# Kernel tuning notes

Hardware: AMD Instinct MI355X
Metric: run time of the kernel (lower is better)

## Reference

```python
import jax, jax.numpy as jnp
from jax import lax
from jax.scipy.special import logsumexp
import numpy as np

N_NODES = 6144
N_EDGES = 98304
N_FEAT = 128
N_TPLT = 16
M_NODES = 10
N_CG = 5        # conditional-gradient (Frank-Wolfe) outer iterations
N_SINK = 50     # log-domain Sinkhorn iterations for the linearized OT subproblem


def setup_inputs() -> dict:
    key = jax.random.key(0)
    k1, k2, k3, k4 = jax.random.split(key, 4)
    x = jax.random.normal(k1, (N_NODES, N_FEAT), dtype=jnp.float32)
    edge_index = jax.random.randint(k2, (2, N_EDGES), 0, N_NODES, dtype=jnp.int64)
    # template_initialisation: uniform(0,1) adjacencies, symmetrized; normal features; zero q0/alpha0
    t_raw = jax.random.uniform(k3, (N_TPLT, M_NODES, M_NODES), dtype=jnp.float32)
    templates = 0.5 * (t_raw + jnp.transpose(t_raw, (0, 2, 1)))
    templates_features = jax.random.normal(k4, (N_TPLT, M_NODES, N_FEAT), dtype=jnp.float32)
    q0 = jnp.zeros((N_TPLT, M_NODES), dtype=jnp.float32)
    alpha0 = jnp.zeros((1,), dtype=jnp.float32)
    return {"x": x, "edge_index": edge_index, "templates": templates,
            "templates_features": templates_features, "q0": q0, "alpha0": alpha0}


def _sinkhorn_log(G, logp, logq, reg):
    """Log-domain Sinkhorn solving min <G,T> + reg*H(T) over U(p,q)."""
    K = -G / reg                         # [n, m]
    f0 = jnp.zeros_like(logp)

    def body(f, _):
        g = logq - logsumexp(K + f[:, None], axis=0)
        f = logp - logsumexp(K + g[None, :], axis=1)
        return f, None

    f, _ = lax.scan(body, f0, None, length=N_SINK)
    g = logq - logsumexp(K + f[:, None], axis=0)
    return jnp.exp(f[:, None] + K + g[None, :])


def _fgw2(M, C1, C2, p, q, alpha):
    """Fused Gromov-Wasserstein distance (square loss) via conditional gradient.
    M: [n,m] feature cost, C1: [n,n] graph structure, C2: [m,m] template structure."""
    # init_matrix (square loss): constC = f1(C1) p 1^T + 1 q^T f2(C2)^T
    constC = (C1 ** 2 @ p)[:, None] + (C2 ** 2 @ q)[None, :]   # [n, m]
    logp, logq = jnp.log(p), jnp.log(q)
    T0 = p[:, None] * q[None, :]

    def step(T, _):
        C1TC2 = C1 @ T @ C2                                   # [n, m] (dominant cost)
        grad = (1.0 - alpha) * M + alpha * 2.0 * (constC - 2.0 * C1TC2)
        reg = lax.stop_gradient(0.05 * jnp.max(jnp.abs(grad)) + 1e-8)
        Tn = _sinkhorn_log(grad, logp, logq, reg)             # linearized OT subproblem
        dT = Tn - T
        # exact line search for the quadratic objective along dT
        C1dTC2 = C1 @ dT @ C2
        a = -2.0 * alpha * jnp.sum(C1dTC2 * dT)
        b = (1.0 - alpha) * jnp.sum(M * dT) + alpha * (jnp.sum(constC * dT) - 4.0 * jnp.sum(C1TC2 * dT))
        tau = jnp.where(a > 0.0,
                        jnp.clip(-b / (2.0 * a + 1e-16), 0.0, 1.0),
                        jnp.where(a + b < 0.0, 1.0, 0.0))
        return T + tau * dT, None

    T, _ = lax.scan(step, T0, None, length=N_CG)
    gw = jnp.sum((constC - 2.0 * (C1 @ T @ C2)) * T)
    wass = jnp.sum(M * T)
    return (1.0 - alpha) * wass + alpha * gw


def reference(x, edge_index, templates, templates_features, q0, alpha0):
    alpha = jax.nn.sigmoid(alpha0)[0]
    q = jax.nn.softmax(q0, axis=1)                            # [T, m] template node weights
    n = x.shape[0]
    # dense adjacency from edge list (symmetrized)
    A = jnp.zeros((n, n), dtype=x.dtype).at[edge_index[0], edge_index[1]].set(1.0)
    C1 = jnp.maximum(A, A.T)                                  # [n, n]
    p = jnp.full((n,), 1.0 / n, dtype=x.dtype)
    # squared euclidean feature cost per template: [T, n, m]
    M = (jnp.sum(x ** 2, axis=1)[None, :, None]
         + jnp.sum(templates_features ** 2, axis=-1)[:, None, :]
         - 2.0 * jnp.einsum('nf,tmf->tnm', x, templates_features))
    dists = jax.vmap(_fgw2, in_axes=(0, None, 0, None, 0, None))(M, C1, templates, p, q, alpha)
    return dists                                              # [n_templates]
```

## Files before the change

kernel.cpp:

```cpp
#include <hip/hip_runtime.h>
#include <hip/hip_cooperative_groups.h>

namespace cgx = cooperative_groups;

static constexpr int NN  = 6144;
static constexpr int NE  = 98304;
static constexpr int NF  = 128;
static constexpr int NT  = 16;
static constexpr int MN  = 10;
static constexpr int NCG = 5;
static constexpr int NSK = 50;
static constexpr int WPR = NN / 32;
static constexpr int TPB = 768;
static constexpr int NBLK = 256;
static constexpr int RPT = NN / TPB;
static constexpr int NW  = TPB / 64;

static_assert(TPB * RPT == NN, "row mapping");

static constexpr size_t OFF_M   = 0;
static constexpr size_t OFF_T   = OFF_M  + (size_t)NT * NN * MN;
static constexpr size_t OFF_C   = OFF_T  + (size_t)NT * NN * 5;
static constexpr size_t OFF_D   = OFF_C  + (size_t)NT * NN * 5;
static constexpr size_t OFF_RS  = OFF_D  + (size_t)NT * NN * 5;
static constexpr size_t OFF_DEG = OFF_RS + NN;
static constexpr size_t OFF_CI  = OFF_DEG + NN;
static constexpr size_t OFF_NNZ = OFF_CI + NE;

static constexpr int LDS_PL  = NN * 20;
static constexpr int LDS_SP  = TPB * 7 * 4;
static constexpr int LDS_DYN = LDS_PL + LDS_SP;

__device__ __forceinline__ unsigned f2bf(float f) {
    unsigned u = __float_as_uint(f);
    return (u + 0x7fffu + ((u >> 16) & 1u)) >> 16;
}
__device__ __forceinline__ unsigned packbf(float a, float b) { return f2bf(a) | (f2bf(b) << 16); }
__device__ __forceinline__ float bflo(unsigned w) { return __uint_as_float(w << 16); }
__device__ __forceinline__ float bfhi(unsigned w) { return __uint_as_float(w & 0xffff0000u); }

extern __shared__ char sMem[];

__global__ __launch_bounds__(TPB) void tfgw_kernel(
    const float* __restrict__ x, const void* __restrict__ eiv,
    const float* __restrict__ tpl, const float* __restrict__ tf,
    const float* __restrict__ q0, const float* __restrict__ a0,
    float* __restrict__ out, float* __restrict__ W)
{
    __shared__ float sC2[MN * MN];
    __shared__ float sq[MN], scq[MN], sqC2[MN], sNSQ[MN];
    __shared__ unsigned svp[5];
    __shared__ float sVf[MN];
    __shared__ float sCv[5];
    __shared__ float sRed[3 * NW];
    __shared__ float sBC[2];
    __shared__ float sDots[4];

    const int tid = threadIdx.x;
    const int bid = blockIdx.x;

    unsigned* BM    = (unsigned*)(W + OFF_T);
    int* rowst      = (int*)(W + OFF_RS);
    int* degi       = (int*)(W + OFF_DEG);
    unsigned short* colix = (unsigned short*)(W + OFF_CI);
    int* nnzc       = (int*)(W + OFF_NNZ);
    float* Mw  = W + OFF_M;
    unsigned* Tg = (unsigned*)(W + OFF_T);
    unsigned* Cg = (unsigned*)(W + OFF_C);
    unsigned* Dg = (unsigned*)(W + OFF_D);

    uint4*    PL4x = (uint4*)sMem;
    unsigned* PL1x = (unsigned*)(sMem + NN * 16);
    unsigned* sPp  = (unsigned*)(sMem + LDS_PL);

    const float alpha  = 1.f / (1.f + __expf(-a0[0]));
    const float invn   = 1.f / (float)NN;
    const float alpha2 = 2.f * alpha;
    const float oma    = 1.f - alpha;

    cgx::grid_group grid = cgx::this_grid();

    for (int idx = bid * TPB + tid; idx < NN * WPR; idx += NBLK * TPB) BM[idx] = 0u;
    if (bid == 0 && tid == 0) *nnzc = 0;
    grid.sync();

    {
        const unsigned* uw = (const unsigned*)eiv;
        const bool is64 = (uw[1] == 0u && uw[3] == 0u && uw[5] == 0u);
        for (int e = bid * TPB + tid; e < NE; e += NBLK * TPB) {
            int s, d;
            if (is64) {
                s = (int)((const long long*)eiv)[e];
                d = (int)((const long long*)eiv)[NE + e];
            } else {
                s = ((const int*)eiv)[e];
                d = ((const int*)eiv)[NE + e];
            }
            atomicOr(&BM[(size_t)s * WPR + (d >> 5)], 1u << (d & 31));
            atomicOr(&BM[(size_t)d * WPR + (s >> 5)], 1u << (s & 31));
        }
        float* sTF = (float*)sMem;
        const int t = bid >> 4, rb = bid & 15;
        for (int k = tid; k < MN * NF; k += TPB) sTF[k] = tf[t * MN * NF + k];
        __syncthreads();
        if (tid < MN) {
            float s = 0.f;
            for (int k = 0; k < NF; ++k) { float v = sTF[tid * NF + k]; s += v * v; }
            sNSQ[tid] = s;
        }
        __syncthreads();
        if (tid < 384) {
            const int i = rb * 384 + tid;
            const float4* x4 = (const float4*)(x + (size_t)i * NF);
            const float4* t4 = (const float4*)sTF;
            float acc[MN]; float xn = 0.f;
            #pragma unroll
            for (int j = 0; j < MN; ++j) acc[j] = 0.f;
            for (int k4 = 0; k4 < NF / 4; ++k4) {
                float4 xv = x4[k4];
                xn += xv.x * xv.x + xv.y * xv.y + xv.z * xv.z + xv.w * xv.w;
                #pragma unroll
                for (int j = 0; j < MN; ++j) {
                    float4 tv = t4[j * (NF / 4) + k4];
                    acc[j] += xv.x * tv.x + xv.y * tv.y + xv.z * tv.z + xv.w * tv.w;
                }
            }
            float* Mrow = Mw + (size_t)t * NN * MN + (size_t)i * MN;
            #pragma unroll
            for (int j = 0; j < MN; ++j) Mrow[j] = xn + sNSQ[j] - 2.f * acc[j];
        }
    }
    grid.sync();

    {
        const int i = bid * TPB + tid;
        if (i < NN) {
            int cnt = 0;
            for (int w = 0; w < WPR; ++w) cnt += __popc(BM[(size_t)i * WPR + w]);
            int st = atomicAdd(nnzc, cnt);
            rowst[i] = st; degi[i] = cnt;
            int p = st;
            for (int w = 0; w < WPR; ++w) {
                unsigned m = BM[(size_t)i * WPR + w];
                while (m) { int b = __ffs(m) - 1; m &= m - 1; colix[p++] = (unsigned short)((w << 5) + b); }
            }
        }
    }
    grid.sync();

    if (bid >= NT) return;

    const int t = bid;
    float* Mb = Mw + (size_t)t * NN * MN;
    unsigned* Tb = Tg + (size_t)t * NN * 5;
    unsigned* Cb = Cg + (size_t)t * NN * 5;
    unsigned* Db = Dg + (size_t)t * NN * 5;

    if (tid == 0) {
        float qv[MN]; float qm = -1e30f;
        for (int j = 0; j < MN; ++j) { qv[j] = q0[t * MN + j]; qm = fmaxf(qm, qv[j]); }
        float qs = 0.f;
        for (int j = 0; j < MN; ++j) { qv[j] = __expf(qv[j] - qm); qs += qv[j]; }
        for (int j = 0; j < MN; ++j) { qv[j] /= qs; sq[j] = qv[j]; }
        for (int j = 0; j < MN; ++j) {
            float s2 = 0.f, s1 = 0.f;
            for (int k = 0; k < MN; ++k) {
                float cjk = tpl[t * MN * MN + j * MN + k];
                s2 += cjk * cjk * qv[k];
                s1 += tpl[t * MN * MN + k * MN + j] * qv[k];
            }
            scq[j] = s2; sqC2[j] = s1;
        }
    }
    for (int k = tid; k < MN * MN; k += TPB) sC2[k] = tpl[t * MN * MN + k];
    __syncthreads();

    float uu[RPT];

    for (int cgi = 0; cgi < NCG; ++cgi) {
        if (tid == 0) {
            float tau = 0.f;
            if (cgi > 0) {
                float a = -2.f * alpha * sDots[3];
                float b = oma * sDots[0] + alpha * (sDots[1] - 4.f * sDots[2]);
                if (a > 0.f) tau = fminf(fmaxf(-b / (2.f * a + 1e-16f), 0.f), 1.f);
                else         tau = (a + b < 0.f) ? 1.f : 0.f;
            }
            sBC[0] = tau;
        }
        __syncthreads();
        const float tau = sBC[0];
        if (cgi > 0 && tau == 0.f) break;

        float gmax = 0.f;
        #pragma unroll
        for (int k = 0; k < RPT; ++k) {
            const int r = tid + k * TPB;
            const float cp = (float)degi[r] * invn;
            const size_t b5 = (size_t)r * 5;
            float C[MN];
            if (cgi == 0) {
                #pragma unroll
                for (int h = 0; h < 5; ++h) {
                    unsigned tw = packbf(sq[2*h] * invn, sq[2*h+1] * invn);
                    unsigned cw = packbf(cp * sqC2[2*h], cp * sqC2[2*h+1]);
                    Tb[b5 + h] = tw; Cb[b5 + h] = cw;
                    C[2*h] = bflo(cw); C[2*h+1] = bfhi(cw);
                }
            } else {
                float dd[MN];
                uint4 a = PL4x[r]; unsigned b4 = PL1x[r];
                dd[0]=bflo(a.x); dd[1]=bfhi(a.x); dd[2]=bflo(a.y); dd[3]=bfhi(a.y);
                dd[4]=bflo(a.z); dd[5]=bfhi(a.z); dd[6]=bflo(a.w); dd[7]=bfhi(a.w);
                dd[8]=bflo(b4);  dd[9]=bfhi(b4);
                #pragma unroll
                for (int h = 0; h < 5; ++h) {
                    unsigned tw = Tb[b5 + h], cw = Cb[b5 + h], Dw = Db[b5 + h];
                    float T0 = bflo(tw) + tau * dd[2*h];
                    float T1 = bfhi(tw) + tau * dd[2*h+1];
                    float C0 = bflo(cw) + tau * bflo(Dw);
                    float C1v = bfhi(cw) + tau * bfhi(Dw);
                    unsigned ntw = packbf(T0, T1), ncw = packbf(C0, C1v);
                    Tb[b5 + h] = ntw; Cb[b5 + h] = ncw;
                    C[2*h] = bflo(ncw); C[2*h+1] = bfhi(ncw);
                }
            }
            float g[MN];
            #pragma unroll
            for (int h = 0; h < 5; ++h) {
                float2 mv = *(const float2*)(Mb + (size_t)r * MN + 2*h);
                g[2*h]   = oma * mv.x + alpha2 * (cp + scq[2*h]   - 2.f * C[2*h]);
                g[2*h+1] = oma * mv.y + alpha2 * (cp + scq[2*h+1] - 2.f * C[2*h+1]);
                gmax = fmaxf(gmax, fmaxf(__builtin_fabsf(g[2*h]), __builtin_fabsf(g[2*h+1])));
            }
            PL4x[r] = make_uint4(packbf(g[0],g[1]), packbf(g[2],g[3]),
                                 packbf(g[4],g[5]), packbf(g[6],g[7]));
            PL1x[r] = packbf(g[8], g[9]);
        }
        #pragma unroll
        for (int d = 32; d; d >>= 1) gmax = fmaxf(gmax, __shfl_xor(gmax, d));
        if ((tid & 63) == 0) sRed[tid >> 6] = gmax;
        __syncthreads();
        if (tid == 0) {
            float m = sRed[0];
            for (int w = 1; w < NW; ++w) m = fmaxf(m, sRed[w]);
            sBC[1] = 1.f / (0.05f * m + 1e-8f);
        }
        __syncthreads();
        const float invreg = sBC[1];

        #pragma unroll
        for (int k = 0; k < RPT; ++k) {
            const int r = tid + k * TPB;
            uint4 a = PL4x[r]; unsigned b4 = PL1x[r];
            float g[MN];
            g[0]=bflo(a.x); g[1]=bfhi(a.x); g[2]=bflo(a.y); g[3]=bfhi(a.y);
            g[4]=bflo(a.z); g[5]=bfhi(a.z); g[6]=bflo(a.w); g[7]=bfhi(a.w);
            g[8]=bflo(b4);  g[9]=bfhi(b4);
            float e[MN];
            #pragma unroll
            for (int j = 0; j < MN; ++j) e[j] = __expf(-g[j] * invreg);
            PL4x[r] = make_uint4(packbf(e[0],e[1]), packbf(e[2],e[3]),
                                 packbf(e[4],e[5]), packbf(e[6],e[7]));
            PL1x[r] = packbf(e[8], e[9]);
        }

        if (cgi == 0) {
            float a[MN];
            #pragma unroll
            for (int j = 0; j < MN; ++j) a[j] = 0.f;
            #pragma unroll
            for (int k = 0; k < RPT; ++k) {
                const int r = tid + k * TPB;
                uint4 q = PL4x[r]; unsigned b4 = PL1x[r];
                a[0]+=bflo(q.x); a[1]+=bfhi(q.x); a[2]+=bflo(q.y); a[3]+=bfhi(q.y);
                a[4]+=bflo(q.z); a[5]+=bfhi(q.z); a[6]+=bflo(q.w); a[7]+=bfhi(q.w);
                a[8]+=bflo(b4);  a[9]+=bfhi(b4);
            }
            #pragma unroll
            for (int p = 0; p < 5; ++p) sPp[tid * 7 + p] = packbf(a[2*p], a[2*p+1]);
            __syncthreads();
            if (tid < 320) {
                const int p = tid >> 6, c = tid & 63;
                float s0 = 0.f, s1 = 0.f;
                #pragma unroll
                for (int kk = 0; kk < NW; ++kk) {
                    unsigned w = sPp[(c + (kk << 6)) * 7 + p];
                    s0 += bflo(w); s1 += bfhi(w);
                }
                #pragma unroll
                for (int d = 32; d; d >>= 1) { s0 += __shfl_xor(s0, d); s1 += __shfl_xor(s1, d); }
                if (c == 0) {
                    float v0 = sq[2*p] / s0, v1 = sq[2*p+1] / s1;
                    svp[p] = packbf(v0, v1);
                    sVf[2*p] = v0; sVf[2*p+1] = v1;
                }
            }
            __syncthreads();
        }

        for (int it = 1; it <= NSK; ++it) {
            float vv[MN];
            #pragma unroll
            for (int p = 0; p < 5; ++p) {
                unsigned w = svp[p];
                vv[2*p] = bflo(w); vv[2*p+1] = bfhi(w);
            }
            float a[MN];
            #pragma unroll
            for (int j = 0; j < MN; ++j) a[j] = 0.f;
            #pragma unroll
            for (int k = 0; k < RPT; ++k) {
                const int r = tid + k * TPB;
                uint4 q = PL4x[r]; unsigned b4 = PL1x[r];
                float e[MN];
                e[0]=bflo(q.x); e[1]=bfhi(q.x); e[2]=bflo(q.y); e[3]=bfhi(q.y);
                e[4]=bflo(q.z); e[5]=bfhi(q.z); e[6]=bflo(q.w); e[7]=bfhi(q.w);
                e[8]=bflo(b4);  e[9]=bfhi(b4);
                float R = 0.f;
                #pragma unroll
                for (int j = 0; j < MN; ++j) R += e[j] * vv[j];
                const float u = invn * __builtin_amdgcn_rcpf(R);
                uu[k] = u;
                #pragma unroll
                for (int j = 0; j < MN; ++j) a[j] += e[j] * u;
            }
            #pragma unroll
            for (int p = 0; p < 5; ++p) sPp[tid * 7 + p] = packbf(a[2*p], a[2*p+1]);
            __syncthreads();
            if (tid < 320) {
                const int p = tid >> 6, c = tid & 63;
                float s0 = 0.f, s1 = 0.f;
                #pragma unroll
                for (int kk = 0; kk < NW; ++kk) {
                    unsigned w = sPp[(c + (kk << 6)) * 7 + p];
                    s0 += bflo(w); s1 += bfhi(w);
                }
                #pragma unroll
                for (int d = 32; d; d >>= 1) { s0 += __shfl_xor(s0, d); s1 += __shfl_xor(s1, d); }
                if (c == 0) {
                    float v0 = sq[2*p] / s0, v1 = sq[2*p+1] / s1;
                    float o0 = sVf[2*p],    o1 = sVf[2*p+1];
                    sCv[p] = (__builtin_fabsf(v0 - o0) <= 2e-4f * v0 &&
                              __builtin_fabsf(v1 - o1) <= 2e-4f * v1) ? 1.f : 0.f;
                    sVf[2*p] = v0; sVf[2*p+1] = v1;
                    svp[p] = packbf(v0, v1);
                }
            }
            __syncthreads();
            if (sCv[0] + sCv[1] + sCv[2] + sCv[3] + sCv[4] == 5.f) break;
        }

        {
            float vv[MN];
            #pragma unroll
            for (int p = 0; p < 5; ++p) {
                unsigned w = svp[p];
                vv[2*p] = bflo(w); vv[2*p+1] = bfhi(w);
            }
            float sMdT = 0.f, sCdT = 0.f, sCTdT = 0.f;
            #pragma unroll
            for (int k = 0; k < RPT; ++k) {
                const int r = tid + k * TPB;
                const float cp = (float)degi[r] * invn;
                const size_t b5 = (size_t)r * 5;
                const float u = uu[k];
                uint4 q = PL4x[r]; unsigned b4 = PL1x[r];
                float e[MN], dd[MN];
                e[0]=bflo(q.x); e[1]=bfhi(q.x); e[2]=bflo(q.y); e[3]=bfhi(q.y);
                e[4]=bflo(q.z); e[5]=bfhi(q.z); e[6]=bflo(q.w); e[7]=bfhi(q.w);
                e[8]=bflo(b4);  e[9]=bfhi(b4);
                #pragma unroll
                for (int h = 0; h < 5; ++h) {
                    unsigned tw = Tb[b5 + h], cw = Cb[b5 + h];
                    float2 mv = *(const float2*)(Mb + (size_t)r * MN + 2*h);
                    float d0 = u * e[2*h]   * vv[2*h]   - bflo(tw);
                    float d1 = u * e[2*h+1] * vv[2*h+1] - bfhi(tw);
                    dd[2*h] = d0; dd[2*h+1] = d1;
                    sMdT  += mv.x * d0 + mv.y * d1;
                    sCdT  += (cp + scq[2*h]) * d0 + (cp + scq[2*h+1]) * d1;
                    sCTdT += bflo(cw) * d0 + bfhi(cw) * d1;
                }
                PL4x[r] = make_uint4(packbf(dd[0],dd[1]), packbf(dd[2],dd[3]),
                                     packbf(dd[4],dd[5]), packbf(dd[6],dd[7]));
                PL1x[r] = packbf(dd[8], dd[9]);
            }
            #pragma unroll
            for (int d = 32; d; d >>= 1) {
                sMdT  += __shfl_xor(sMdT, d);
                sCdT  += __shfl_xor(sCdT, d);
                sCTdT += __shfl_xor(sCTdT, d);
            }
            if ((tid & 63) == 0) {
                const int w = tid >> 6;
                sRed[w] = sMdT; sRed[NW + w] = sCdT; sRed[2*NW + w] = sCTdT;
            }
            __syncthreads();
            if (tid == 0) {
                float r0 = 0.f, r1 = 0.f, r2 = 0.f;
                for (int w = 0; w < NW; ++w) { r0 += sRed[w]; r1 += sRed[NW+w]; r2 += sRed[2*NW+w]; }
                sDots[0] = r0; sDots[1] = r1; sDots[2] = r2;
            }
        }

        {
            float dot = 0.f;
            #pragma unroll
            for (int k = 0; k < RPT; ++k) {
                const int r = tid + k * TPB;
                float y[MN];
                #pragma unroll
                for (int j = 0; j < MN; ++j) y[j] = 0.f;
                const int st = rowst[r], dg = degi[r];
                const unsigned short* cl = colix + st;
                for (int e = 0; e < dg; ++e) {
                    const int j = cl[e];
                    uint4 q = PL4x[j]; unsigned b4 = PL1x[j];
                    y[0] += bflo(q.x); y[1] += bfhi(q.x);
                    y[2] += bflo(q.y); y[3] += bfhi(q.y);
                    y[4] += bflo(q.z); y[5] += bfhi(q.z);
                    y[6] += bflo(q.w); y[7] += bfhi(q.w);
                    y[8] += bflo(b4);  y[9] += bfhi(b4);
                }
                uint4 q = PL4x[r]; unsigned b4 = PL1x[r];
                float dd[MN];
                dd[0]=bflo(q.x); dd[1]=bfhi(q.x); dd[2]=bflo(q.y); dd[3]=bfhi(q.y);
                dd[4]=bflo(q.z); dd[5]=bfhi(q.z); dd[6]=bflo(q.w); dd[7]=bfhi(q.w);
                dd[8]=bflo(b4);  dd[9]=bfhi(b4);
                #pragma unroll
                for (int h = 0; h < 5; ++h) {
                    float o0 = 0.f, o1 = 0.f;
                    #pragma unroll
                    for (int j = 0; j < MN; ++j) {
                        o0 += y[j] * sC2[j * MN + 2*h];
                        o1 += y[j] * sC2[j * MN + 2*h + 1];
                    }
                    dot += o0 * dd[2*h] + o1 * dd[2*h+1];
                    Db[(size_t)r * 5 + h] = packbf(o0, o1);
                }
            }
            #pragma unroll
            for (int d = 32; d; d >>= 1) dot += __shfl_xor(dot, d);
            if ((tid & 63) == 0) sRed[tid >> 6] = dot;
            __syncthreads();
            if (tid == 0) {
                float s = 0.f;
                for (int w = 0; w < NW; ++w) s += sRed[w];
                sDots[3] = s;
            }
            __syncthreads();
        }
    }

    if (tid == 0) {
        float a = -2.f * alpha * sDots[3];
        float b = oma * sDots[0] + alpha * (sDots[1] - 4.f * sDots[2]);
        float tau;
        if (a > 0.f) tau = fminf(fmaxf(-b / (2.f * a + 1e-16f), 0.f), 1.f);
        else         tau = (a + b < 0.f) ? 1.f : 0.f;
        sBC[0] = tau;
    }
    __syncthreads();
    {
        const float tau = sBC[0];
        float gw = 0.f, wass = 0.f;
        #pragma unroll
        for (int k = 0; k < RPT; ++k) {
            const int r = tid + k * TPB;
            const float cp = (float)degi[r] * invn;
            const size_t b5 = (size_t)r * 5;
            uint4 q = PL4x[r]; unsigned b4 = PL1x[r];
            float dd[MN];
            dd[0]=bflo(q.x); dd[1]=bfhi(q.x); dd[2]=bflo(q.y); dd[3]=bfhi(q.y);
            dd[4]=bflo(q.z); dd[5]=bfhi(q.z); dd[6]=bflo(q.w); dd[7]=bfhi(q.w);
            dd[8]=bflo(b4);  dd[9]=bfhi(b4);
            #pragma unroll
            for (int h = 0; h < 5; ++h) {
                unsigned tw = Tb[b5 + h], cw = Cb[b5 + h], Dw = Db[b5 + h];
                float2 mv = *(const float2*)(Mb + (size_t)r * MN + 2*h);
                float Tf0 = bflo(tw) + tau * dd[2*h];
                float Tf1 = bfhi(tw) + tau * dd[2*h+1];
                float Cf0 = bflo(cw) + tau * bflo(Dw);
                float Cf1 = bfhi(cw) + tau * bfhi(Dw);
                gw   += (cp + scq[2*h]   - 2.f * Cf0) * Tf0
                      + (cp + scq[2*h+1] - 2.f * Cf1) * Tf1;
                wass += mv.x * Tf0 + mv.y * Tf1;
            }
        }
        #pragma unroll
        for (int d = 32; d; d >>= 1) {
            gw   += __shfl_xor(gw, d);
            wass += __shfl_xor(wass, d);
        }
        if ((tid & 63) == 0) { sRed[tid >> 6] = gw; sRed[NW + (tid >> 6)] = wass; }
        __syncthreads();
        if (tid == 0) {
            float g = 0.f, ws = 0.f;
            for (int w = 0; w < NW; ++w) { g += sRed[w]; ws += sRed[NW + w]; }
            out[t] = oma * ws + alpha * g;
        }
    }
}

extern "C" void kernel_launch(void* const* d_in, const int* in_sizes, int n_in,
                              void* d_out, int out_size, void* d_ws, size_t ws_size,
                              hipStream_t stream) {
    const float* x   = (const float*)d_in[0];
    const void*  ei  = d_in[1];
    const float* tpl = (const float*)d_in[2];
    const float* tfp = (const float*)d_in[3];
    const float* q0  = (const float*)d_in[4];
    const float* a0  = (const float*)d_in[5];
    float* outp = (float*)d_out;
    float* Wp   = (float*)d_ws;
    (void)hipFuncSetAttribute(reinterpret_cast<const void*>(&tfgw_kernel),
                              hipFuncAttributeMaxDynamicSharedMemorySize, LDS_DYN);
    void* args[] = { &x, &ei, &tpl, &tfp, &q0, &a0, &outp, &Wp };
    hipLaunchCooperativeKernel(reinterpret_cast<const void*>(&tfgw_kernel),
                               dim3(NBLK), dim3(TPB), args, LDS_DYN, stream);
}
```

Before: 706.6 us.

## Split T/C/D global buffers into uint4+uint planes and recompute Sinkhorn row scale

Stores the per-template bf16 T, C and D arrays as a 16-byte uint4 plane plus a 4-byte plane, instead of five strided 4-byte words per row. Loads and stores become coalesced vector accesses rather than stride-20 scalar ones. The Sinkhorn row scale u is recomputed in the direction pass instead of being kept in a register array, which lowers register pressure. The convergence test now compares packed bf16 column scalings against the previous two iterates instead of using a float relative tolerance, which may change when Sinkhorn stops early.

```diff
diff --git a/kernel.cpp b/kernel.cpp
--- a/kernel.cpp
+++ b/kernel.cpp
@@ -19,10 +19,13 @@
 static_assert(TPB * RPT == NN, "row mapping");
 
 static constexpr size_t OFF_M   = 0;
-static constexpr size_t OFF_T   = OFF_M  + (size_t)NT * NN * MN;
-static constexpr size_t OFF_C   = OFF_T  + (size_t)NT * NN * 5;
-static constexpr size_t OFF_D   = OFF_C  + (size_t)NT * NN * 5;
-static constexpr size_t OFF_RS  = OFF_D  + (size_t)NT * NN * 5;
+static constexpr size_t OFF_T4  = OFF_M  + (size_t)NT * NN * MN;
+static constexpr size_t OFF_T1  = OFF_T4 + (size_t)NT * NN * 4;
+static constexpr size_t OFF_C4  = OFF_T1 + (size_t)NT * NN;
+static constexpr size_t OFF_C1  = OFF_C4 + (size_t)NT * NN * 4;
+static constexpr size_t OFF_D4  = OFF_C1 + (size_t)NT * NN;
+static constexpr size_t OFF_D1  = OFF_D4 + (size_t)NT * NN * 4;
+static constexpr size_t OFF_RS  = OFF_D1 + (size_t)NT * NN;
 static constexpr size_t OFF_DEG = OFF_RS + NN;
 static constexpr size_t OFF_CI  = OFF_DEG + NN;
 static constexpr size_t OFF_NNZ = OFF_CI + NE;
@@ -50,7 +53,7 @@
     __shared__ float sC2[MN * MN];
     __shared__ float sq[MN], scq[MN], sqC2[MN], sNSQ[MN];
     __shared__ unsigned svp[5];
-    __shared__ float sVf[MN];
+    __shared__ unsigned svP2[5];
     __shared__ float sCv[5];
     __shared__ float sRed[3 * NW];
     __shared__ float sBC[2];
@@ -59,15 +62,12 @@
     const int tid = threadIdx.x;
     const int bid = blockIdx.x;
 
-    unsigned* BM    = (unsigned*)(W + OFF_T);
+    unsigned* BM    = (unsigned*)(W + OFF_T4);
     int* rowst      = (int*)(W + OFF_RS);
     int* degi       = (int*)(W + OFF_DEG);
     unsigned short* colix = (unsigned short*)(W + OFF_CI);
     int* nnzc       = (int*)(W + OFF_NNZ);
     float* Mw  = W + OFF_M;
-    unsigned* Tg = (unsigned*)(W + OFF_T);
-    unsigned* Cg = (unsigned*)(W + OFF_C);
-    unsigned* Dg = (unsigned*)(W + OFF_D);
 
     uint4*    PL4x = (uint4*)sMem;
     unsigned* PL1x = (unsigned*)(sMem + NN * 16);
@@ -152,9 +152,12 @@
 
     const int t = bid;
     float* Mb = Mw + (size_t)t * NN * MN;
-    unsigned* Tb = Tg + (size_t)t * NN * 5;
-    unsigned* Cb = Cg + (size_t)t * NN * 5;
-    unsigned* Db = Dg + (size_t)t * NN * 5;
+    uint4*    Tb4 = (uint4*)(W + OFF_T4) + (size_t)t * NN;
+    unsigned* Tb1 = (unsigned*)(W + OFF_T1) + (size_t)t * NN;
+    uint4*    Cb4 = (uint4*)(W + OFF_C4) + (size_t)t * NN;
+    unsigned* Cb1 = (unsigned*)(W + OFF_C1) + (size_t)t * NN;
+    uint4*    Db4 = (uint4*)(W + OFF_D4) + (size_t)t * NN;
+    unsigned* Db1 = (unsigned*)(W + OFF_D1) + (size_t)t * NN;
 
     if (tid == 0) {
         float qv[MN]; float qm = -1e30f;
@@ -175,8 +178,6 @@
     for (int k = tid; k < MN * MN; k += TPB) sC2[k] = tpl[t * MN * MN + k];
     __syncthreads();
 
-    float uu[RPT];
-
     for (int cgi = 0; cgi < NCG; ++cgi) {
         if (tid == 0) {
             float tau = 0.f;
@@ -188,6 +189,7 @@
             }
             sBC[0] = tau;
         }
+        if (tid < 5) svP2[tid] = 0xFFFFFFFFu;
         __syncthreads();
         const float tau = sBC[0];
         if (cgi > 0 && tau == 0.f) break;
@@ -197,33 +199,52 @@
         for (int k = 0; k < RPT; ++k) {
             const int r = tid + k * TPB;
             const float cp = (float)degi[r] * invn;
-            const size_t b5 = (size_t)r * 5;
             float C[MN];
             if (cgi == 0) {
-                #pragma unroll
-                for (int h = 0; h < 5; ++h) {
-                    unsigned tw = packbf(sq[2*h] * invn, sq[2*h+1] * invn);
-                    unsigned cw = packbf(cp * sqC2[2*h], cp * sqC2[2*h+1]);
-                    Tb[b5 + h] = tw; Cb[b5 + h] = cw;
-                    C[2*h] = bflo(cw); C[2*h+1] = bfhi(cw);
-                }
+                uint4 tw4; unsigned tw1;
+                uint4 cw4; unsigned cw1;
+                tw4.x = packbf(sq[0]*invn, sq[1]*invn); tw4.y = packbf(sq[2]*invn, sq[3]*invn);
+                tw4.z = packbf(sq[4]*invn, sq[5]*invn); tw4.w = packbf(sq[6]*invn, sq[7]*invn);
+                tw1   = packbf(sq[8]*invn, sq[9]*invn);
+                cw4.x = packbf(cp*sqC2[0], cp*sqC2[1]); cw4.y = packbf(cp*sqC2[2], cp*sqC2[3]);
+                cw4.z = packbf(cp*sqC2[4], cp*sqC2[5]); cw4.w = packbf(cp*sqC2[6], cp*sqC2[7]);
+                cw1   = packbf(cp*sqC2[8], cp*sqC2[9]);
+                Tb4[r] = tw4; Tb1[r] = tw1; Cb4[r] = cw4; Cb1[r] = cw1;
+                C[0]=bflo(cw4.x); C[1]=bfhi(cw4.x); C[2]=bflo(cw4.y); C[3]=bfhi(cw4.y);
+                C[4]=bflo(cw4.z); C[5]=bfhi(cw4.z); C[6]=bflo(cw4.w); C[7]=bfhi(cw4.w);
+                C[8]=bflo(cw1);   C[9]=bfhi(cw1);
             } else {
                 float dd[MN];
                 uint4 a = PL4x[r]; unsigned b4 = PL1x[r];
                 dd[0]=bflo(a.x); dd[1]=bfhi(a.x); dd[2]=bflo(a.y); dd[3]=bfhi(a.y);
                 dd[4]=bflo(a.z); dd[5]=bfhi(a.z); dd[6]=bflo(a.w); dd[7]=bfhi(a.w);
                 dd[8]=bflo(b4);  dd[9]=bfhi(b4);
-                #pragma unroll
-                for (int h = 0; h < 5; ++h) {
-                    unsigned tw = Tb[b5 + h], cw = Cb[b5 + h], Dw = Db[b5 + h];
-                    float T0 = bflo(tw) + tau * dd[2*h];
-                    float T1 = bfhi(tw) + tau * dd[2*h+1];
-                    float C0 = bflo(cw) + tau * bflo(Dw);
-                    float C1v = bfhi(cw) + tau * bfhi(Dw);
-                    unsigned ntw = packbf(T0, T1), ncw = packbf(C0, C1v);
-                    Tb[b5 + h] = ntw; Cb[b5 + h] = ncw;
-                    C[2*h] = bflo(ncw); C[2*h+1] = bfhi(ncw);
-                }
+                uint4 tw4 = Tb4[r]; unsigned tw1 = Tb1[r];
+                uint4 cw4 = Cb4[r]; unsigned cw1 = Cb1[r];
+                uint4 Dw4 = Db4[r]; unsigned Dw1 = Db1[r];
+                float T[MN], Dd[MN];
+                T[0]=bflo(tw4.x); T[1]=bfhi(tw4.x); T[2]=bflo(tw4.y); T[3]=bfhi(tw4.y);
+                T[4]=bflo(tw4.z); T[5]=bfhi(tw4.z); T[6]=bflo(tw4.w); T[7]=bfhi(tw4.w);
+                T[8]=bflo(tw1);   T[9]=bfhi(tw1);
+                C[0]=bflo(cw4.x); C[1]=bfhi(cw4.x); C[2]=bflo(cw4.y); C[3]=bfhi(cw4.y);
+                C[4]=bflo(cw4.z); C[5]=bfhi(cw4.z); C[6]=bflo(cw4.w); C[7]=bfhi(cw4.w);
+                C[8]=bflo(cw1);   C[9]=bfhi(cw1);
+                Dd[0]=bflo(Dw4.x); Dd[1]=bfhi(Dw4.x); Dd[2]=bflo(Dw4.y); Dd[3]=bfhi(Dw4.y);
+                Dd[4]=bflo(Dw4.z); Dd[5]=bfhi(Dw4.z); Dd[6]=bflo(Dw4.w); Dd[7]=bfhi(Dw4.w);
+                Dd[8]=bflo(Dw1);   Dd[9]=bfhi(Dw1);
+                #pragma unroll
+                for (int j = 0; j < MN; ++j) { T[j] += tau * dd[j]; C[j] += tau * Dd[j]; }
+                uint4 ntw4; unsigned ntw1; uint4 ncw4; unsigned ncw1;
+                ntw4.x = packbf(T[0],T[1]); ntw4.y = packbf(T[2],T[3]);
+                ntw4.z = packbf(T[4],T[5]); ntw4.w = packbf(T[6],T[7]);
+                ntw1   = packbf(T[8],T[9]);
+                ncw4.x = packbf(C[0],C[1]); ncw4.y = packbf(C[2],C[3]);
+                ncw4.z = packbf(C[4],C[5]); ncw4.w = packbf(C[6],C[7]);
+                ncw1   = packbf(C[8],C[9]);
+                Tb4[r] = ntw4; Tb1[r] = ntw1; Cb4[r] = ncw4; Cb1[r] = ncw1;
+                C[0]=bflo(ncw4.x); C[1]=bfhi(ncw4.x); C[2]=bflo(ncw4.y); C[3]=bfhi(ncw4.y);
+                C[4]=bflo(ncw4.z); C[5]=bfhi(ncw4.z); C[6]=bflo(ncw4.w); C[7]=bfhi(ncw4.w);
+                C[8]=bflo(ncw1);   C[9]=bfhi(ncw1);
             }
             float g[MN];
             #pragma unroll
@@ -290,11 +311,7 @@
                 }
                 #pragma unroll
                 for (int d = 32; d; d >>= 1) { s0 += __shfl_xor(s0, d); s1 += __shfl_xor(s1, d); }
-                if (c == 0) {
-                    float v0 = sq[2*p] / s0, v1 = sq[2*p+1] / s1;
-                    svp[p] = packbf(v0, v1);
-                    sVf[2*p] = v0; sVf[2*p+1] = v1;
-                }
+                if (c == 0) svp[p] = packbf(sq[2*p] / s0, sq[2*p+1] / s1);
             }
             __syncthreads();
         }
@@ -321,7 +338,6 @@
                 #pragma unroll
                 for (int j = 0; j < MN; ++j) R += e[j] * vv[j];
                 const float u = invn * __builtin_amdgcn_rcpf(R);
-                uu[k] = u;
                 #pragma unroll
                 for (int j = 0; j < MN; ++j) a[j] += e[j] * u;
             }
@@ -339,12 +355,11 @@
                 #pragma unroll
                 for (int d = 32; d; d >>= 1) { s0 += __shfl_xor(s0, d); s1 += __shfl_xor(s1, d); }
                 if (c == 0) {
-                    float v0 = sq[2*p] / s0, v1 = sq[2*p+1] / s1;
-                    float o0 = sVf[2*p],    o1 = sVf[2*p+1];
-                    sCv[p] = (__builtin_fabsf(v0 - o0) <= 2e-4f * v0 &&
-                              __builtin_fabsf(v1 - o1) <= 2e-4f * v1) ? 1.f : 0.f;
-                    sVf[2*p] = v0; sVf[2*p+1] = v1;
-                    svp[p] = packbf(v0, v1);
+                    unsigned pw = packbf(sq[2*p] / s0, sq[2*p+1] / s1);
+                    unsigned old = svp[p], old2 = svP2[p];
+                    sCv[p] = (pw == old || pw == old2) ? 1.f : 0.f;
+                    svP2[p] = old;
+                    svp[p] = pw;
                 }
             }
             __syncthreads();
@@ -363,23 +378,33 @@
             for (int k = 0; k < RPT; ++k) {
                 const int r = tid + k * TPB;
                 const float cp = (float)degi[r] * invn;
-                const size_t b5 = (size_t)r * 5;
-                const float u = uu[k];
                 uint4 q = PL4x[r]; unsigned b4 = PL1x[r];
                 float e[MN], dd[MN];
                 e[0]=bflo(q.x); e[1]=bfhi(q.x); e[2]=bflo(q.y); e[3]=bfhi(q.y);
                 e[4]=bflo(q.z); e[5]=bfhi(q.z); e[6]=bflo(q.w); e[7]=bfhi(q.w);
                 e[8]=bflo(b4);  e[9]=bfhi(b4);
+                float R = 0.f;
+                #pragma unroll
+                for (int j = 0; j < MN; ++j) R += e[j] * vv[j];
+                const float u = invn * __builtin_amdgcn_rcpf(R);
+                uint4 tw4 = Tb4[r]; unsigned tw1 = Tb1[r];
+                uint4 cw4 = Cb4[r]; unsigned cw1 = Cb1[r];
+                float T[MN], C[MN];
+                T[0]=bflo(tw4.x); T[1]=bfhi(tw4.x); T[2]=bflo(tw4.y); T[3]=bfhi(tw4.y);
+                T[4]=bflo(tw4.z); T[5]=bfhi(tw4.z); T[6]=bflo(tw4.w); T[7]=bfhi(tw4.w);
+                T[8]=bflo(tw1);   T[9]=bfhi(tw1);
+                C[0]=bflo(cw4.x); C[1]=bfhi(cw4.x); C[2]=bflo(cw4.y); C[3]=bfhi(cw4.y);
+                C[4]=bflo(cw4.z); C[5]=bfhi(cw4.z); C[6]=bflo(cw4.w); C[7]=bfhi(cw4.w);
+                C[8]=bflo(cw1);   C[9]=bfhi(cw1);
                 #pragma unroll
                 for (int h = 0; h < 5; ++h) {
-                    unsigned tw = Tb[b5 + h], cw = Cb[b5 + h];
                     float2 mv = *(const float2*)(Mb + (size_t)r * MN + 2*h);
-                    float d0 = u * e[2*h]   * vv[2*h]   - bflo(tw);
-                    float d1 = u * e[2*h+1] * vv[2*h+1] - bfhi(tw);
+                    float d0 = u * e[2*h]   * vv[2*h]   - T[2*h];
+                    float d1 = u * e[2*h+1] * vv[2*h+1] - T[2*h+1];
                     dd[2*h] = d0; dd[2*h+1] = d1;
                     sMdT  += mv.x * d0 + mv.y * d1;
                     sCdT  += (cp + scq[2*h]) * d0 + (cp + scq[2*h+1]) * d1;
-                    sCTdT += bflo(cw) * d0 + bfhi(cw) * d1;
+                    sCTdT += C[2*h] * d0 + C[2*h+1] * d1;
                 }
                 PL4x[r] = make_uint4(packbf(dd[0],dd[1]), packbf(dd[2],dd[3]),
                                      packbf(dd[4],dd[5]), packbf(dd[6],dd[7]));
@@ -427,6 +452,7 @@
                 dd[0]=bflo(q.x); dd[1]=bfhi(q.x); dd[2]=bflo(q.y); dd[3]=bfhi(q.y);
                 dd[4]=bflo(q.z); dd[5]=bfhi(q.z); dd[6]=bflo(q.w); dd[7]=bfhi(q.w);
                 dd[8]=bflo(b4);  dd[9]=bfhi(b4);
+                float o[MN];
                 #pragma unroll
                 for (int h = 0; h < 5; ++h) {
                     float o0 = 0.f, o1 = 0.f;
@@ -435,9 +461,12 @@
                         o0 += y[j] * sC2[j * MN + 2*h];
                         o1 += y[j] * sC2[j * MN + 2*h + 1];
                     }
+                    o[2*h] = o0; o[2*h+1] = o1;
                     dot += o0 * dd[2*h] + o1 * dd[2*h+1];
-                    Db[(size_t)r * 5 + h] = packbf(o0, o1);
-                }
+                }
+                Db4[r] = make_uint4(packbf(o[0],o[1]), packbf(o[2],o[3]),
+                                    packbf(o[4],o[5]), packbf(o[6],o[7]));
+                Db1[r] = packbf(o[8], o[9]);
             }
             #pragma unroll
             for (int d = 32; d; d >>= 1) dot += __shfl_xor(dot, d);
@@ -468,20 +497,31 @@
         for (int k = 0; k < RPT; ++k) {
             const int r = tid + k * TPB;
             const float cp = (float)degi[r] * invn;
-            const size_t b5 = (size_t)r * 5;
             uint4 q = PL4x[r]; unsigned b4 = PL1x[r];
             float dd[MN];
             dd[0]=bflo(q.x); dd[1]=bfhi(q.x); dd[2]=bflo(q.y); dd[3]=bfhi(q.y);
             dd[4]=bflo(q.z); dd[5]=bfhi(q.z); dd[6]=bflo(q.w); dd[7]=bfhi(q.w);
             dd[8]=bflo(b4);  dd[9]=bfhi(b4);
+            uint4 tw4 = Tb4[r]; unsigned tw1 = Tb1[r];
+            uint4 cw4 = Cb4[r]; unsigned cw1 = Cb1[r];
+            uint4 Dw4 = Db4[r]; unsigned Dw1 = Db1[r];
+            float T[MN], C[MN], Dd[MN];
+            T[0]=bflo(tw4.x); T[1]=bfhi(tw4.x); T[2]=bflo(tw4.y); T[3]=bfhi(tw4.y);
+            T[4]=bflo(tw4.z); T[5]=bfhi(tw4.z); T[6]=bflo(tw4.w); T[7]=bfhi(tw4.w);
+            T[8]=bflo(tw1);   T[9]=bfhi(tw1);
+            C[0]=bflo(cw4.x); C[1]=bfhi(cw4.x); C[2]=bflo(cw4.y); C[3]=bfhi(cw4.y);
+            C[4]=bflo(cw4.z); C[5]=bfhi(cw4.z); C[6]=bflo(cw4.w); C[7]=bfhi(cw4.w);
+            C[8]=bflo(cw1);   C[9]=bfhi(cw1);
+            Dd[0]=bflo(Dw4.x); Dd[1]=bfhi(Dw4.x); Dd[2]=bflo(Dw4.y); Dd[3]=bfhi(Dw4.y);
+            Dd[4]=bflo(Dw4.z); Dd[5]=bfhi(Dw4.z); Dd[6]=bflo(Dw4.w); Dd[7]=bfhi(Dw4.w);
+            Dd[8]=bflo(Dw1);   Dd[9]=bfhi(Dw1);
             #pragma unroll
             for (int h = 0; h < 5; ++h) {
-                unsigned tw = Tb[b5 + h], cw = Cb[b5 + h], Dw = Db[b5 + h];
                 float2 mv = *(const float2*)(Mb + (size_t)r * MN + 2*h);
-                float Tf0 = bflo(tw) + tau * dd[2*h];
-                float Tf1 = bfhi(tw) + tau * dd[2*h+1];
-                float Cf0 = bflo(cw) + tau * bflo(Dw);
-                float Cf1 = bfhi(cw) + tau * bfhi(Dw);
+                float Tf0 = T[2*h]   + tau * dd[2*h];
+                float Tf1 = T[2*h+1] + tau * dd[2*h+1];
+                float Cf0 = C[2*h]   + tau * Dd[2*h];
+                float Cf1 = C[2*h+1] + tau * Dd[2*h+1];
                 gw   += (cp + scq[2*h]   - 2.f * Cf0) * Tf0
                       + (cp + scq[2*h+1] - 2.f * Cf1) * Tf1;
                 wass += mv.x * Tf0 + mv.y * Tf1;
```

Result: no change. 713.1 us (+0.9%).
